# Optimization experiments

Measured on AMD Instinct MI355X. Metric: run time of the kernel, lower is better.

Reference implementation:

```python
import jax, jax.numpy as jnp
import numpy as np

N_NODES = 100000
N_EDGES = 1600000
D_IN = 64
D_OUT = 64


def setup_inputs() -> dict:
    key = jax.random.key(0)
    k1, k2, k3, k4, k5, k6 = jax.random.split(key, 6)
    x = jax.random.normal(k1, (N_NODES, D_IN), dtype=jnp.float32)
    edge_index = jax.random.randint(k2, (2, N_EDGES), 0, N_NODES, dtype=jnp.int64)
    edge_weight = jax.random.uniform(k3, (N_EDGES,), dtype=jnp.float32)
    scale = 1.0 / np.sqrt(D_IN)
    W0 = jax.random.normal(k4, (D_IN, D_OUT), dtype=jnp.float32) * scale
    W1 = jax.random.normal(k5, (D_IN, D_OUT), dtype=jnp.float32) * scale
    b = jax.random.normal(k6, (D_OUT,), dtype=jnp.float32) * 0.01
    return {"x": x, "edge_index": edge_index, "edge_weight": edge_weight,
            "W0": W0, "W1": W1, "b": b}


def reference(x, edge_index, edge_weight, W0, W1, b):
    # ChebConv K=2 with default lambda_max=2.0, sym normalization:
    # L_hat = 2L/lambda_max - I = -D^{-1/2} A D^{-1/2}
    N = x.shape[0]
    row, col = edge_index[0], edge_index[1]
    deg = jax.ops.segment_sum(edge_weight, row, num_segments=N)  # [N]
    deg_safe = jnp.where(deg > 0, deg, 1.0)
    dinv = jnp.where(deg > 0, jax.lax.rsqrt(deg_safe), 0.0)
    norm = -dinv[row] * edge_weight * dinv[col]  # [E], L_hat edge weights
    # Tx_1[i] = sum_{e: col_e = i} norm_e * x[row_e]
    Tx1 = jax.ops.segment_sum(norm[:, None] * x[row], col, num_segments=N)
    # out = lin0(Tx_0) + lin1(Tx_1) + bias
    return x @ W0 + Tx1 @ W1 + b
```

## Files before the change

### kernel.cpp

```cpp
#include <hip/hip_runtime.h>

#define N_NODES 100000
#define N_EDGES 1600000
#define D 64
#define NB 128
#define EPB (N_EDGES / NB)
#define NBUCK 3125
#define NBUCK_PAD 3136
#define NGRP 98
#define CAP 1024
#define AST 68

__device__ __forceinline__ unsigned bf16rne(float f) {
    unsigned u = __float_as_uint(f);
    return (u + 0x7FFFu + ((u >> 16) & 1u)) >> 16;
}
__global__ __launch_bounds__(256) void tobf16_kernel(const float* __restrict__ x,
                                                     ushort* __restrict__ xh) {
    int i = (blockIdx.x * 256 + threadIdx.x) * 8;
    float4 a = *(const float4*)(x + i);
    float4 b = *(const float4*)(x + i + 4);
    uint4 o;
    o.x = bf16rne(a.x) | (bf16rne(a.y) << 16);
    o.y = bf16rne(a.z) | (bf16rne(a.w) << 16);
    o.z = bf16rne(b.x) | (bf16rne(b.y) << 16);
    o.w = bf16rne(b.z) | (bf16rne(b.w) << 16);
    *(uint4*)(xh + i) = o;
}

__global__ __launch_bounds__(512) void count_kernel(const int* __restrict__ row,
                                                    const int* __restrict__ col,
                                                    int* __restrict__ matC,
                                                    int* __restrict__ matR) {
    __shared__ int cC[NBUCK_PAD];
    __shared__ int cR[NBUCK_PAD];
    int t = threadIdx.x;
    for (int j = t; j < NBUCK_PAD; j += 512) { cC[j] = 0; cR[j] = 0; }
    __syncthreads();
    int base = blockIdx.x * EPB;
    for (int i = t; i < EPB; i += 512) {
        int e = base + i;
        atomicAdd(&cC[col[e] >> 5], 1);
        atomicAdd(&cR[row[e] >> 5], 1);
    }
    __syncthreads();
    int* mc = matC + (size_t)blockIdx.x * NBUCK_PAD;
    int* mr = matR + (size_t)blockIdx.x * NBUCK_PAD;
    for (int j = t; j < NBUCK_PAD; j += 512) { mc[j] = cC[j]; mr[j] = cR[j]; }
}

__global__ __launch_bounds__(256) void blockscan_kernel(int* __restrict__ matC,
                                                        int* __restrict__ matR,
                                                        int* __restrict__ totalsC,
                                                        int* __restrict__ totalsR) {
    int which = blockIdx.x / NGRP;
    int grp   = blockIdx.x % NGRP;
    int* mat    = which ? matR : matC;
    int* totals = which ? totalsR : totalsC;
    int j0 = grp * 32;
    __shared__ int tile[NB][33];
    int t = threadIdx.x;
    int r = t >> 1;
    int h = t & 1;
    {
        const int* src = mat + (size_t)r * NBUCK_PAD + j0 + h * 16;
        int4 v0 = *(const int4*)(src + 0);
        int4 v1 = *(const int4*)(src + 4);
        int4 v2 = *(const int4*)(src + 8);
        int4 v3 = *(const int4*)(src + 12);
        int cb = h * 16;
        tile[r][cb+0]=v0.x;  tile[r][cb+1]=v0.y;  tile[r][cb+2]=v0.z;  tile[r][cb+3]=v0.w;
        tile[r][cb+4]=v1.x;  tile[r][cb+5]=v1.y;  tile[r][cb+6]=v1.z;  tile[r][cb+7]=v1.w;
        tile[r][cb+8]=v2.x;  tile[r][cb+9]=v2.y;  tile[r][cb+10]=v2.z; tile[r][cb+11]=v2.w;
        tile[r][cb+12]=v3.x; tile[r][cb+13]=v3.y; tile[r][cb+14]=v3.z; tile[r][cb+15]=v3.w;
    }
    __syncthreads();
    int g = t >> 3;
    int l = t & 7;
    int rows0 = l * 16;
    int vals[16];
    int s = 0;
    #pragma unroll
    for (int i = 0; i < 16; ++i) { vals[i] = tile[rows0 + i][g]; s += vals[i]; }
    int inc = s;
    #pragma unroll
    for (int d = 1; d < 8; d <<= 1) {
        int u = __shfl_up(inc, d, 8);
        if (l >= d) inc += u;
    }
    int excl = inc - s;
    #pragma unroll
    for (int i = 0; i < 16; ++i) { int e2 = excl; excl += vals[i]; tile[rows0 + i][g] = e2; }
    if (l == 7) totals[j0 + g] = inc;
    __syncthreads();
    {
        int* dst = mat + (size_t)r * NBUCK_PAD + j0 + h * 16;
        int cb = h * 16;
        int4 v0 = make_int4(tile[r][cb+0],  tile[r][cb+1],  tile[r][cb+2],  tile[r][cb+3]);
        int4 v1 = make_int4(tile[r][cb+4],  tile[r][cb+5],  tile[r][cb+6],  tile[r][cb+7]);
        int4 v2 = make_int4(tile[r][cb+8],  tile[r][cb+9],  tile[r][cb+10], tile[r][cb+11]);
        int4 v3 = make_int4(tile[r][cb+12], tile[r][cb+13], tile[r][cb+14], tile[r][cb+15]);
        *(int4*)(dst + 0)  = v0;
        *(int4*)(dst + 4)  = v1;
        *(int4*)(dst + 8)  = v2;
        *(int4*)(dst + 12) = v3;
    }
}

__global__ __launch_bounds__(256) void totscan_kernel(const int* __restrict__ totalsC,
                                                      int* __restrict__ bstartC,
                                                      const int* __restrict__ totalsR,
                                                      int* __restrict__ bstartR) {
    const int* tot = blockIdx.x ? totalsR : totalsC;
    int* bst       = blockIdx.x ? bstartR : bstartC;
    const int CH = (NBUCK_PAD + 255) / 256;
    __shared__ int lds[256];
    int t = threadIdx.x;
    int local[CH];
    int s = 0;
    for (int i = 0; i < CH; ++i) {
        int idx = t * CH + i;
        local[i] = (idx < NBUCK_PAD) ? tot[idx] : 0;
        s += local[i];
    }
    lds[t] = s;
    __syncthreads();
    for (int off = 1; off < 256; off <<= 1) {
        int u = (t >= off) ? lds[t - off] : 0;
        __syncthreads();
        lds[t] += u;
        __syncthreads();
    }
    int excl = (t > 0) ? lds[t - 1] : 0;
    for (int i = 0; i < CH; ++i) {
        int idx = t * CH + i;
        if (idx < NBUCK_PAD) bst[idx] = excl;
        excl += local[i];
    }
}

__global__ __launch_bounds__(512) void scatter_kernel(const int* __restrict__ row,
                                                      const int* __restrict__ col,
                                                      const float* __restrict__ w,
                                                      const int* __restrict__ matC,
                                                      const int* __restrict__ matR,
                                                      const int* __restrict__ bstartC,
                                                      const int* __restrict__ bstartR,
                                                      unsigned* __restrict__ crecs,
                                                      unsigned* __restrict__ rrecs) {
    __shared__ int cursC[NBUCK];
    __shared__ int cursR[NBUCK];
    int t = threadIdx.x;
    const int* offC = matC + (size_t)blockIdx.x * NBUCK_PAD;
    const int* offR = matR + (size_t)blockIdx.x * NBUCK_PAD;
    for (int j = t; j < NBUCK; j += 512) {
        cursC[j] = bstartC[j] + offC[j];
        cursR[j] = bstartR[j] + offR[j];
    }
    __syncthreads();
    int base = blockIdx.x * EPB;
    for (int i = t; i < EPB; i += 512) {
        int e = base + i;
        int r = row[e];
        int c = col[e];
        float we = w[e];
        unsigned wq = (unsigned)min(1023, (int)(we * 1024.f + 0.5f));
        int pC = atomicAdd(&cursC[c >> 5], 1);
        crecs[pC] = ((unsigned)r << 15) | ((unsigned)(c & 31) << 10) | wq;
        int pR = atomicAdd(&cursR[r >> 5], 1);
        rrecs[pR] = (__float_as_uint(we) & ~31u) | (unsigned)(r & 31);
    }
}

__global__ __launch_bounds__(256) void deg_kernel(const unsigned* __restrict__ rrecs,
                                                  const int* __restrict__ bstartR,
                                                  const int* __restrict__ totalsR,
                                                  float* __restrict__ dinv) {
    __shared__ float acc[32];
    int t = threadIdx.x;
    int b = blockIdx.x;
    if (t < 32) acc[t] = 0.f;
    __syncthreads();
    int base = bstartR[b];
    int cnt  = totalsR[b];
    for (int i = t; i < cnt; i += 256) {
        unsigned v = rrecs[base + i];
        atomicAdd(&acc[v & 31u], __uint_as_float(v & ~31u));
    }
    __syncthreads();
    if (t < 32) {
        float d = acc[t];
        dinv[b * 32 + t] = d > 0.f ? rsqrtf(d) : 0.f;
    }
}

#define FMA_BF16(e, u)                                                         \
    do { float cc = __int_as_float((e).y);                                     \
        acc0.x += cc * __uint_as_float((u).x << 16);                           \
        acc0.y += cc * __uint_as_float((u).x & 0xFFFF0000u);                   \
        acc0.z += cc * __uint_as_float((u).y << 16);                           \
        acc0.w += cc * __uint_as_float((u).y & 0xFFFF0000u);                   \
        acc1.x += cc * __uint_as_float((u).z << 16);                           \
        acc1.y += cc * __uint_as_float((u).z & 0xFFFF0000u);                   \
        acc1.z += cc * __uint_as_float((u).w << 16);                           \
        acc1.w += cc * __uint_as_float((u).w & 0xFFFF0000u);                   \
    } while (0)

__global__ __launch_bounds__(256) void gather_out_kernel(
        const unsigned* __restrict__ crecs, const int* __restrict__ bstartC,
        const int* __restrict__ totalsC, const float* __restrict__ dinv,
        const ushort* __restrict__ xh, const float* __restrict__ x,
        const float* __restrict__ W0, const float* __restrict__ W1,
        const float* __restrict__ bias, float* __restrict__ out) {
    __shared__ __align__(16) char smemA[32 * AST * 4];
    __shared__ __align__(16) char smemB[32 * AST * 4];
    __shared__ int cnt32[32];
    __shared__ int start32[32];
    __shared__ int cur32[32];
    int2*  srt = (int2*)smemA;
    float* xs  = (float*)smemA;
    float* ts  = (float*)smemB;

    int tid = threadIdx.x;
    int b   = blockIdx.x;
    int n0  = b * 32;
    int g   = tid >> 3;
    int j   = tid & 7;

    int base = bstartC[b];
    int cnt  = totalsC[b];

    float4 acc0 = make_float4(0.f, 0.f, 0.f, 0.f);
    float4 acc1 = make_float4(0.f, 0.f, 0.f, 0.f);
    const ushort* xhj = xh + (j << 3);

    for (int cb = 0; cb < cnt; cb += CAP) {
        int m = min(CAP, cnt - cb);
        if (tid < 32) cnt32[tid] = 0;
        __syncthreads();
        for (int i = tid; i < m; i += 256)
            atomicAdd(&cnt32[(crecs[base + cb + i] >> 10) & 31u], 1);
        __syncthreads();
        if (tid < 32) {
            int v = cnt32[tid];
            int inc = v;
            #pragma unroll
            for (int d = 1; d < 32; d <<= 1) {
                int u = __shfl_up(inc, d, 32);
                if (tid >= d) inc += u;
            }
            start32[tid] = inc - v;
            cur32[tid]   = inc - v;
        }
        __syncthreads();
        for (int i = tid; i < m; i += 256) {
            unsigned u = crecs[base + cb + i];
            int r = u >> 15;
            float cf = (float)(u & 1023u) * (1.f / 1024.f) * dinv[r];
            int p = atomicAdd(&cur32[(u >> 10) & 31u], 1);
            srt[p] = make_int2(r, __float_as_int(cf));
        }
        __syncthreads();
        int ks = start32[g];
        int ke = cur32[g];
        int k = ks;
        for (; k + 3 < ke; k += 4) {
            int2 e0 = srt[k + 0];
            int2 e1 = srt[k + 1];
            int2 e2 = srt[k + 2];
            int2 e3 = srt[k + 3];
            uint4 u0 = *(const uint4*)(xhj + ((size_t)e0.x << 6));
            uint4 u1 = *(const uint4*)(xhj + ((size_t)e1.x << 6));
            uint4 u2 = *(const uint4*)(xhj + ((size_t)e2.x << 6));
            uint4 u3 = *(const uint4*)(xhj + ((size_t)e3.x << 6));
            FMA_BF16(e0, u0);
            FMA_BF16(e1, u1);
            FMA_BF16(e2, u2);
            FMA_BF16(e3, u3);
        }
        for (; k < ke; ++k) {
            int2 e0 = srt[k];
            uint4 u0 = *(const uint4*)(xhj + ((size_t)e0.x << 6));
            FMA_BF16(e0, u0);
        }
        __syncthreads();
    }

    float dn = -dinv[n0 + g];
    float* tp = ts + g * AST + (j << 3);
    *(float4*)tp       = make_float4(dn * acc0.x, dn * acc0.y, dn * acc0.z, dn * acc0.w);
    *(float4*)(tp + 4) = make_float4(dn * acc1.x, dn * acc1.y, dn * acc1.z, dn * acc1.w);
    for (int i = tid; i < 512; i += 256) {
        int nn = i >> 4;
        int kk = (i & 15) << 2;
        *(float4*)&xs[nn * AST + kk] = *(const float4*)(x + (size_t)n0 * D + i * 4);
    }
    __syncthreads();

    int jl = j << 3;
    float4 o0 = *(const float4*)(bias + jl);
    float4 o1 = *(const float4*)(bias + jl + 4);
    for (int k = 0; k < D; k += 4) {
        float4 av = *(const float4*)&xs[g * AST + k];
        float4 tv = *(const float4*)&ts[g * AST + k];
        #pragma unroll
        for (int u = 0; u < 4; ++u) {
            float a = (u == 0) ? av.x : (u == 1) ? av.y : (u == 2) ? av.z : av.w;
            float t = (u == 0) ? tv.x : (u == 1) ? tv.y : (u == 2) ? tv.z : tv.w;
            const float4 w00 = *(const float4*)(W0 + (size_t)(k + u) * D + jl);
            const float4 w01 = *(const float4*)(W0 + (size_t)(k + u) * D + jl + 4);
            const float4 w10 = *(const float4*)(W1 + (size_t)(k + u) * D + jl);
            const float4 w11 = *(const float4*)(W1 + (size_t)(k + u) * D + jl + 4);
            o0.x += a * w00.x + t * w10.x;
            o0.y += a * w00.y + t * w10.y;
            o0.z += a * w00.z + t * w10.z;
            o0.w += a * w00.w + t * w10.w;
            o1.x += a * w01.x + t * w11.x;
            o1.y += a * w01.y + t * w11.y;
            o1.z += a * w01.z + t * w11.z;
            o1.w += a * w01.w + t * w11.w;
        }
    }
    float* op = out + (size_t)(n0 + g) * D + jl;
    *(float4*)op       = o0;
    *(float4*)(op + 4) = o1;
}

extern "C" void kernel_launch(void* const* d_in, const int* in_sizes, int n_in,
                              void* d_out, int out_size, void* d_ws, size_t ws_size,
                              hipStream_t stream) {
    const float* x    = (const float*)d_in[0];
    const int*   eidx = (const int*)d_in[1];
    const float* ew   = (const float*)d_in[2];
    const float* W0   = (const float*)d_in[3];
    const float* W1   = (const float*)d_in[4];
    const float* b    = (const float*)d_in[5];
    float* out = (float*)d_out;

    const int* row = eidx;
    const int* col = eidx + N_EDGES;

    unsigned* crecs   = (unsigned*)d_ws;
    unsigned* rrecs   = crecs + N_EDGES;
    int*      matC    = (int*)(rrecs + N_EDGES);
    int*      matR    = matC + (size_t)NB * NBUCK_PAD;
    int*      totalsC = matR + (size_t)NB * NBUCK_PAD;
    int*      bstartC = totalsC + NBUCK_PAD;
    int*      totalsR = bstartC + NBUCK_PAD;
    int*      bstartR = totalsR + NBUCK_PAD;
    float*    dinv    = (float*)(bstartR + NBUCK_PAD);
    ushort*   xh      = (ushort*)(dinv + N_NODES);

    tobf16_kernel    <<<N_NODES * D / (256 * 8), 256, 0, stream>>>(x, xh);
    count_kernel     <<<NB, 512, 0, stream>>>(row, col, matC, matR);
    blockscan_kernel <<<2 * NGRP, 256, 0, stream>>>(matC, matR, totalsC, totalsR);
    totscan_kernel   <<<2, 256, 0, stream>>>(totalsC, bstartC, totalsR, bstartR);
    scatter_kernel   <<<NB, 512, 0, stream>>>(row, col, ew, matC, matR,
                                              bstartC, bstartR, crecs, rrecs);
    deg_kernel       <<<NBUCK, 256, 0, stream>>>(rrecs, bstartR, totalsR, dinv);
    gather_out_kernel<<<NBUCK, 256, 0, stream>>>(crecs, bstartC, totalsC, dinv,
                                                 xh, x, W0, W1, b, out);
}
```

Before: 284.3 us.

## Replace count/scan bucket sort with fixed-capacity atomic buckets and atomic degree

Removes the count, two-level scan and row-bucketed scatter/degree kernels. Edges are appended with global atomics into fixed-capacity buckets (512 slots per 16 destination nodes), and degrees are accumulated with global float atomics followed by a small rsqrt kernel. The gather kernel shrinks to 16-node blocks of 128 threads and stages records in shared memory in one pass instead of a chunk loop. This cuts kernel launches and the extra passes over the edge list, but any bucket receiving more than 512 edges silently drops the excess. The float atomics also make the degree sums order-dependent.

```diff
diff --git a/kernel.cpp b/kernel.cpp
--- a/kernel.cpp
+++ b/kernel.cpp
@@ -3,12 +3,10 @@
 #define N_NODES 100000
 #define N_EDGES 1600000
 #define D 64
-#define NB 128
-#define EPB (N_EDGES / NB)
-#define NBUCK 3125
-#define NBUCK_PAD 3136
-#define NGRP 98
-#define CAP 1024
+#define BSZ 16
+#define NBUCK 6250
+#define NBUCK_PAD 6272
+#define CAPB 512
 #define AST 68
 
 __device__ __forceinline__ unsigned bf16rne(float f) {
@@ -16,8 +14,13 @@
     return (u + 0x7FFFu + ((u >> 16) & 1u)) >> 16;
 }
 __global__ __launch_bounds__(256) void tobf16_kernel(const float* __restrict__ x,
-                                                     ushort* __restrict__ xh) {
-    int i = (blockIdx.x * 256 + threadIdx.x) * 8;
+                                                     ushort* __restrict__ xh,
+                                                     float* __restrict__ deg,
+                                                     int* __restrict__ bcnt) {
+    int id = blockIdx.x * 256 + threadIdx.x;
+    if (id < N_NODES) deg[id] = 0.f;
+    if (id < NBUCK) bcnt[id] = 0;
+    int i = id * 8;
     float4 a = *(const float4*)(x + i);
     float4 b = *(const float4*)(x + i + 4);
     uint4 o;
@@ -28,170 +31,35 @@
     *(uint4*)(xh + i) = o;
 }
 
-__global__ __launch_bounds__(512) void count_kernel(const int* __restrict__ row,
-                                                    const int* __restrict__ col,
-                                                    int* __restrict__ matC,
-                                                    int* __restrict__ matR) {
-    __shared__ int cC[NBUCK_PAD];
-    __shared__ int cR[NBUCK_PAD];
-    int t = threadIdx.x;
-    for (int j = t; j < NBUCK_PAD; j += 512) { cC[j] = 0; cR[j] = 0; }
-    __syncthreads();
-    int base = blockIdx.x * EPB;
-    for (int i = t; i < EPB; i += 512) {
-        int e = base + i;
-        atomicAdd(&cC[col[e] >> 5], 1);
-        atomicAdd(&cR[row[e] >> 5], 1);
-    }
-    __syncthreads();
-    int* mc = matC + (size_t)blockIdx.x * NBUCK_PAD;
-    int* mr = matR + (size_t)blockIdx.x * NBUCK_PAD;
-    for (int j = t; j < NBUCK_PAD; j += 512) { mc[j] = cC[j]; mr[j] = cR[j]; }
-}
-
-__global__ __launch_bounds__(256) void blockscan_kernel(int* __restrict__ matC,
-                                                        int* __restrict__ matR,
-                                                        int* __restrict__ totalsC,
-                                                        int* __restrict__ totalsR) {
-    int which = blockIdx.x / NGRP;
-    int grp   = blockIdx.x % NGRP;
-    int* mat    = which ? matR : matC;
-    int* totals = which ? totalsR : totalsC;
-    int j0 = grp * 32;
-    __shared__ int tile[NB][33];
-    int t = threadIdx.x;
-    int r = t >> 1;
-    int h = t & 1;
-    {
-        const int* src = mat + (size_t)r * NBUCK_PAD + j0 + h * 16;
-        int4 v0 = *(const int4*)(src + 0);
-        int4 v1 = *(const int4*)(src + 4);
-        int4 v2 = *(const int4*)(src + 8);
-        int4 v3 = *(const int4*)(src + 12);
-        int cb = h * 16;
-        tile[r][cb+0]=v0.x;  tile[r][cb+1]=v0.y;  tile[r][cb+2]=v0.z;  tile[r][cb+3]=v0.w;
-        tile[r][cb+4]=v1.x;  tile[r][cb+5]=v1.y;  tile[r][cb+6]=v1.z;  tile[r][cb+7]=v1.w;
-        tile[r][cb+8]=v2.x;  tile[r][cb+9]=v2.y;  tile[r][cb+10]=v2.z; tile[r][cb+11]=v2.w;
-        tile[r][cb+12]=v3.x; tile[r][cb+13]=v3.y; tile[r][cb+14]=v3.z; tile[r][cb+15]=v3.w;
-    }
-    __syncthreads();
-    int g = t >> 3;
-    int l = t & 7;
-    int rows0 = l * 16;
-    int vals[16];
-    int s = 0;
-    #pragma unroll
-    for (int i = 0; i < 16; ++i) { vals[i] = tile[rows0 + i][g]; s += vals[i]; }
-    int inc = s;
-    #pragma unroll
-    for (int d = 1; d < 8; d <<= 1) {
-        int u = __shfl_up(inc, d, 8);
-        if (l >= d) inc += u;
-    }
-    int excl = inc - s;
-    #pragma unroll
-    for (int i = 0; i < 16; ++i) { int e2 = excl; excl += vals[i]; tile[rows0 + i][g] = e2; }
-    if (l == 7) totals[j0 + g] = inc;
-    __syncthreads();
-    {
-        int* dst = mat + (size_t)r * NBUCK_PAD + j0 + h * 16;
-        int cb = h * 16;
-        int4 v0 = make_int4(tile[r][cb+0],  tile[r][cb+1],  tile[r][cb+2],  tile[r][cb+3]);
-        int4 v1 = make_int4(tile[r][cb+4],  tile[r][cb+5],  tile[r][cb+6],  tile[r][cb+7]);
-        int4 v2 = make_int4(tile[r][cb+8],  tile[r][cb+9],  tile[r][cb+10], tile[r][cb+11]);
-        int4 v3 = make_int4(tile[r][cb+12], tile[r][cb+13], tile[r][cb+14], tile[r][cb+15]);
-        *(int4*)(dst + 0)  = v0;
-        *(int4*)(dst + 4)  = v1;
-        *(int4*)(dst + 8)  = v2;
-        *(int4*)(dst + 12) = v3;
-    }
-}
-
-__global__ __launch_bounds__(256) void totscan_kernel(const int* __restrict__ totalsC,
-                                                      int* __restrict__ bstartC,
-                                                      const int* __restrict__ totalsR,
-                                                      int* __restrict__ bstartR) {
-    const int* tot = blockIdx.x ? totalsR : totalsC;
-    int* bst       = blockIdx.x ? bstartR : bstartC;
-    const int CH = (NBUCK_PAD + 255) / 256;
-    __shared__ int lds[256];
-    int t = threadIdx.x;
-    int local[CH];
-    int s = 0;
-    for (int i = 0; i < CH; ++i) {
-        int idx = t * CH + i;
-        local[i] = (idx < NBUCK_PAD) ? tot[idx] : 0;
-        s += local[i];
-    }
-    lds[t] = s;
-    __syncthreads();
-    for (int off = 1; off < 256; off <<= 1) {
-        int u = (t >= off) ? lds[t - off] : 0;
-        __syncthreads();
-        lds[t] += u;
-        __syncthreads();
-    }
-    int excl = (t > 0) ? lds[t - 1] : 0;
-    for (int i = 0; i < CH; ++i) {
-        int idx = t * CH + i;
-        if (idx < NBUCK_PAD) bst[idx] = excl;
-        excl += local[i];
-    }
-}
-
-__global__ __launch_bounds__(512) void scatter_kernel(const int* __restrict__ row,
+__global__ __launch_bounds__(256) void scatter_kernel(const int* __restrict__ row,
                                                       const int* __restrict__ col,
                                                       const float* __restrict__ w,
-                                                      const int* __restrict__ matC,
-                                                      const int* __restrict__ matR,
-                                                      const int* __restrict__ bstartC,
-                                                      const int* __restrict__ bstartR,
-                                                      unsigned* __restrict__ crecs,
-                                                      unsigned* __restrict__ rrecs) {
-    __shared__ int cursC[NBUCK];
-    __shared__ int cursR[NBUCK];
-    int t = threadIdx.x;
-    const int* offC = matC + (size_t)blockIdx.x * NBUCK_PAD;
-    const int* offR = matR + (size_t)blockIdx.x * NBUCK_PAD;
-    for (int j = t; j < NBUCK; j += 512) {
-        cursC[j] = bstartC[j] + offC[j];
-        cursR[j] = bstartR[j] + offR[j];
-    }
-    __syncthreads();
-    int base = blockIdx.x * EPB;
-    for (int i = t; i < EPB; i += 512) {
-        int e = base + i;
-        int r = row[e];
-        int c = col[e];
-        float we = w[e];
-        unsigned wq = (unsigned)min(1023, (int)(we * 1024.f + 0.5f));
-        int pC = atomicAdd(&cursC[c >> 5], 1);
-        crecs[pC] = ((unsigned)r << 15) | ((unsigned)(c & 31) << 10) | wq;
-        int pR = atomicAdd(&cursR[r >> 5], 1);
-        rrecs[pR] = (__float_as_uint(we) & ~31u) | (unsigned)(r & 31);
-    }
-}
-
-__global__ __launch_bounds__(256) void deg_kernel(const unsigned* __restrict__ rrecs,
-                                                  const int* __restrict__ bstartR,
-                                                  const int* __restrict__ totalsR,
-                                                  float* __restrict__ dinv) {
-    __shared__ float acc[32];
-    int t = threadIdx.x;
-    int b = blockIdx.x;
-    if (t < 32) acc[t] = 0.f;
-    __syncthreads();
-    int base = bstartR[b];
-    int cnt  = totalsR[b];
-    for (int i = t; i < cnt; i += 256) {
-        unsigned v = rrecs[base + i];
-        atomicAdd(&acc[v & 31u], __uint_as_float(v & ~31u));
-    }
-    __syncthreads();
-    if (t < 32) {
-        float d = acc[t];
-        dinv[b * 32 + t] = d > 0.f ? rsqrtf(d) : 0.f;
-    }
+                                                      float* __restrict__ deg,
+                                                      int* __restrict__ bcnt,
+                                                      unsigned* __restrict__ crecs) {
+    int e = blockIdx.x * 256 + threadIdx.x;
+    int r = row[e];
+    int c = col[e];
+    float we = w[e];
+    atomicAdd(&deg[r], we);
+    unsigned wq = (unsigned)min(1023, (int)(we * 1024.f + 0.5f));
+    int b = c >> 4;
+    int p = atomicAdd(&bcnt[b], 1);
+    if (p < CAPB)
+        crecs[((size_t)b << 9) + p] = ((unsigned)r << 14) | ((unsigned)(c & 15) << 10) | wq;
+}
+
+__global__ __launch_bounds__(256) void dinv_kernel(const float* __restrict__ deg,
+                                                   float* __restrict__ dinv) {
+    int i = (blockIdx.x * 256 + threadIdx.x) * 4;
+    if (i >= N_NODES) return;
+    float4 d = *(const float4*)(deg + i);
+    float4 o;
+    o.x = d.x > 0.f ? rsqrtf(d.x) : 0.f;
+    o.y = d.y > 0.f ? rsqrtf(d.y) : 0.f;
+    o.z = d.z > 0.f ? rsqrtf(d.z) : 0.f;
+    o.w = d.w > 0.f ? rsqrtf(d.w) : 0.f;
+    *(float4*)(dinv + i) = o;
 }
 
 #define FMA_BF16(e, u)                                                         \
@@ -206,91 +74,92 @@
         acc1.w += cc * __uint_as_float((u).w & 0xFFFF0000u);                   \
     } while (0)
 
-__global__ __launch_bounds__(256) void gather_out_kernel(
-        const unsigned* __restrict__ crecs, const int* __restrict__ bstartC,
-        const int* __restrict__ totalsC, const float* __restrict__ dinv,
-        const ushort* __restrict__ xh, const float* __restrict__ x,
-        const float* __restrict__ W0, const float* __restrict__ W1,
-        const float* __restrict__ bias, float* __restrict__ out) {
-    __shared__ __align__(16) char smemA[32 * AST * 4];
-    __shared__ __align__(16) char smemB[32 * AST * 4];
-    __shared__ int cnt32[32];
-    __shared__ int start32[32];
-    __shared__ int cur32[32];
-    int2*  srt = (int2*)smemA;
-    float* xs  = (float*)smemA;
-    float* ts  = (float*)smemB;
+__global__ __launch_bounds__(128, 8) void gather_out_kernel(
+        const unsigned* __restrict__ crecs, const int* __restrict__ bcnt,
+        const float* __restrict__ dinv, const ushort* __restrict__ xh,
+        const float* __restrict__ x, const float* __restrict__ W0,
+        const float* __restrict__ W1, const float* __restrict__ bias,
+        float* __restrict__ out) {
+    __shared__ __align__(16) char smemA[BSZ * AST * 4];
+    __shared__ __align__(16) char smemB[BSZ * AST * 4];
+    __shared__ int cnt16[16];
+    __shared__ int start16[16];
+    __shared__ int cur16[16];
+    int2*     srt = (int2*)smemA;
+    float*    xs  = (float*)smemA;
+    unsigned* stg = (unsigned*)smemB;
+    float*    ts  = (float*)smemB;
 
     int tid = threadIdx.x;
     int b   = blockIdx.x;
-    int n0  = b * 32;
+    int n0  = b * BSZ;
     int g   = tid >> 3;
     int j   = tid & 7;
 
-    int base = bstartC[b];
-    int cnt  = totalsC[b];
+    size_t base = (size_t)b * CAPB;
+    int cnt = min(bcnt[b], CAPB);
+
+    if (tid < 16) cnt16[tid] = 0;
+    __syncthreads();
+    for (int i = tid; i < cnt; i += 128) {
+        unsigned u = crecs[base + i];
+        stg[i] = u;
+        atomicAdd(&cnt16[(u >> 10) & 15u], 1);
+    }
+    __syncthreads();
+    if (tid < 16) {
+        int v = cnt16[tid];
+        int inc = v;
+        #pragma unroll
+        for (int d = 1; d < 16; d <<= 1) {
+            int u = __shfl_up(inc, d, 16);
+            if (tid >= d) inc += u;
+        }
+        start16[tid] = inc - v;
+        cur16[tid]   = inc - v;
+    }
+    __syncthreads();
+    for (int i = tid; i < cnt; i += 128) {
+        unsigned u = stg[i];
+        int r = u >> 14;
+        float cf = (float)(u & 1023u) * (1.f / 1024.f) * dinv[r];
+        int p = atomicAdd(&cur16[(u >> 10) & 15u], 1);
+        srt[p] = make_int2(r, __float_as_int(cf));
+    }
+    __syncthreads();
 
     float4 acc0 = make_float4(0.f, 0.f, 0.f, 0.f);
     float4 acc1 = make_float4(0.f, 0.f, 0.f, 0.f);
     const ushort* xhj = xh + (j << 3);
-
-    for (int cb = 0; cb < cnt; cb += CAP) {
-        int m = min(CAP, cnt - cb);
-        if (tid < 32) cnt32[tid] = 0;
-        __syncthreads();
-        for (int i = tid; i < m; i += 256)
-            atomicAdd(&cnt32[(crecs[base + cb + i] >> 10) & 31u], 1);
-        __syncthreads();
-        if (tid < 32) {
-            int v = cnt32[tid];
-            int inc = v;
-            #pragma unroll
-            for (int d = 1; d < 32; d <<= 1) {
-                int u = __shfl_up(inc, d, 32);
-                if (tid >= d) inc += u;
-            }
-            start32[tid] = inc - v;
-            cur32[tid]   = inc - v;
-        }
-        __syncthreads();
-        for (int i = tid; i < m; i += 256) {
-            unsigned u = crecs[base + cb + i];
-            int r = u >> 15;
-            float cf = (float)(u & 1023u) * (1.f / 1024.f) * dinv[r];
-            int p = atomicAdd(&cur32[(u >> 10) & 31u], 1);
-            srt[p] = make_int2(r, __float_as_int(cf));
-        }
-        __syncthreads();
-        int ks = start32[g];
-        int ke = cur32[g];
-        int k = ks;
-        for (; k + 3 < ke; k += 4) {
-            int2 e0 = srt[k + 0];
-            int2 e1 = srt[k + 1];
-            int2 e2 = srt[k + 2];
-            int2 e3 = srt[k + 3];
-            uint4 u0 = *(const uint4*)(xhj + ((size_t)e0.x << 6));
-            uint4 u1 = *(const uint4*)(xhj + ((size_t)e1.x << 6));
-            uint4 u2 = *(const uint4*)(xhj + ((size_t)e2.x << 6));
-            uint4 u3 = *(const uint4*)(xhj + ((size_t)e3.x << 6));
-            FMA_BF16(e0, u0);
-            FMA_BF16(e1, u1);
-            FMA_BF16(e2, u2);
-            FMA_BF16(e3, u3);
-        }
-        for (; k < ke; ++k) {
-            int2 e0 = srt[k];
-            uint4 u0 = *(const uint4*)(xhj + ((size_t)e0.x << 6));
-            FMA_BF16(e0, u0);
-        }
-        __syncthreads();
-    }
+    int ks = start16[g];
+    int ke = cur16[g];
+    int k = ks;
+    for (; k + 3 < ke; k += 4) {
+        int2 e0 = srt[k + 0];
+        int2 e1 = srt[k + 1];
+        int2 e2 = srt[k + 2];
+        int2 e3 = srt[k + 3];
+        uint4 u0 = *(const uint4*)(xhj + ((size_t)e0.x << 6));
+        uint4 u1 = *(const uint4*)(xhj + ((size_t)e1.x << 6));
+        uint4 u2 = *(const uint4*)(xhj + ((size_t)e2.x << 6));
+        uint4 u3 = *(const uint4*)(xhj + ((size_t)e3.x << 6));
+        FMA_BF16(e0, u0);
+        FMA_BF16(e1, u1);
+        FMA_BF16(e2, u2);
+        FMA_BF16(e3, u3);
+    }
+    for (; k < ke; ++k) {
+        int2 e0 = srt[k];
+        uint4 u0 = *(const uint4*)(xhj + ((size_t)e0.x << 6));
+        FMA_BF16(e0, u0);
+    }
+    __syncthreads();
 
     float dn = -dinv[n0 + g];
     float* tp = ts + g * AST + (j << 3);
     *(float4*)tp       = make_float4(dn * acc0.x, dn * acc0.y, dn * acc0.z, dn * acc0.w);
     *(float4*)(tp + 4) = make_float4(dn * acc1.x, dn * acc1.y, dn * acc1.z, dn * acc1.w);
-    for (int i = tid; i < 512; i += 256) {
+    for (int i = tid; i < 256; i += 128) {
         int nn = i >> 4;
         int kk = (i & 15) << 2;
         *(float4*)&xs[nn * AST + kk] = *(const float4*)(x + (size_t)n0 * D + i * 4);
@@ -300,17 +169,17 @@
     int jl = j << 3;
     float4 o0 = *(const float4*)(bias + jl);
     float4 o1 = *(const float4*)(bias + jl + 4);
-    for (int k = 0; k < D; k += 4) {
-        float4 av = *(const float4*)&xs[g * AST + k];
-        float4 tv = *(const float4*)&ts[g * AST + k];
+    for (int k2 = 0; k2 < D; k2 += 4) {
+        float4 av = *(const float4*)&xs[g * AST + k2];
+        float4 tv = *(const float4*)&ts[g * AST + k2];
         #pragma unroll
         for (int u = 0; u < 4; ++u) {
             float a = (u == 0) ? av.x : (u == 1) ? av.y : (u == 2) ? av.z : av.w;
             float t = (u == 0) ? tv.x : (u == 1) ? tv.y : (u == 2) ? tv.z : tv.w;
-            const float4 w00 = *(const float4*)(W0 + (size_t)(k + u) * D + jl);
-            const float4 w01 = *(const float4*)(W0 + (size_t)(k + u) * D + jl + 4);
-            const float4 w10 = *(const float4*)(W1 + (size_t)(k + u) * D + jl);
-            const float4 w11 = *(const float4*)(W1 + (size_t)(k + u) * D + jl + 4);
+            const float4 w00 = *(const float4*)(W0 + (size_t)(k2 + u) * D + jl);
+            const float4 w01 = *(const float4*)(W0 + (size_t)(k2 + u) * D + jl + 4);
+            const float4 w10 = *(const float4*)(W1 + (size_t)(k2 + u) * D + jl);
+            const float4 w11 = *(const float4*)(W1 + (size_t)(k2 + u) * D + jl + 4);
             o0.x += a * w00.x + t * w10.x;
             o0.y += a * w00.y + t * w10.y;
             o0.z += a * w00.z + t * w10.z;
@@ -340,24 +209,14 @@
     const int* row = eidx;
     const int* col = eidx + N_EDGES;
 
-    unsigned* crecs   = (unsigned*)d_ws;
-    unsigned* rrecs   = crecs + N_EDGES;
-    int*      matC    = (int*)(rrecs + N_EDGES);
-    int*      matR    = matC + (size_t)NB * NBUCK_PAD;
-    int*      totalsC = matR + (size_t)NB * NBUCK_PAD;
-    int*      bstartC = totalsC + NBUCK_PAD;
-    int*      totalsR = bstartC + NBUCK_PAD;
-    int*      bstartR = totalsR + NBUCK_PAD;
-    float*    dinv    = (float*)(bstartR + NBUCK_PAD);
-    ushort*   xh      = (ushort*)(dinv + N_NODES);
-
-    tobf16_kernel    <<<N_NODES * D / (256 * 8), 256, 0, stream>>>(x, xh);
-    count_kernel     <<<NB, 512, 0, stream>>>(row, col, matC, matR);
-    blockscan_kernel <<<2 * NGRP, 256, 0, stream>>>(matC, matR, totalsC, totalsR);
-    totscan_kernel   <<<2, 256, 0, stream>>>(totalsC, bstartC, totalsR, bstartR);
-    scatter_kernel   <<<NB, 512, 0, stream>>>(row, col, ew, matC, matR,
-                                              bstartC, bstartR, crecs, rrecs);
-    deg_kernel       <<<NBUCK, 256, 0, stream>>>(rrecs, bstartR, totalsR, dinv);
-    gather_out_kernel<<<NBUCK, 256, 0, stream>>>(crecs, bstartC, totalsC, dinv,
-                                                 xh, x, W0, W1, b, out);
-}
+    unsigned* crecs = (unsigned*)d_ws;
+    float*    deg   = (float*)(crecs + (size_t)NBUCK * CAPB);
+    float*    dinv  = deg + N_NODES;
+    int*      bcnt  = (int*)(dinv + N_NODES);
+    ushort*   xh    = (ushort*)(bcnt + NBUCK_PAD);
+
+    tobf16_kernel    <<<N_NODES * D / (256 * 8), 256, 0, stream>>>(x, xh, deg, bcnt);
+    scatter_kernel   <<<N_EDGES / 256, 256, 0, stream>>>(row, col, ew, deg, bcnt, crecs);
+    dinv_kernel      <<<(N_NODES / 4 + 255) / 256, 256, 0, stream>>>(deg, dinv);
+    gather_out_kernel<<<NBUCK, 128, 0, stream>>>(crecs, bcnt, dinv, xh, x, W0, W1, b, out);
+}
```

After: 376.0 us. +32.2%, slower.

## Compute degree via global atomics into four replicas instead of row bucket sort

Applied to the files above, without the earlier changes.

Drops the row-side bucket counting, scan, record scatter and per-bucket degree reduction. Degree is now accumulated with global float atomicAdd into four replicated arrays chosen by block index; the arrays are zeroed inside the bf16 conversion kernel and summed plus rsqrt'd in a small new kernel. This removes the second radix-style pass over all edges and its record traffic, at the cost of 1.6M contended global atomics and nondeterministic float summation order.

```diff
diff --git a/kernel.cpp b/kernel.cpp
--- a/kernel.cpp
+++ b/kernel.cpp
@@ -16,8 +16,11 @@
     return (u + 0x7FFFu + ((u >> 16) & 1u)) >> 16;
 }
 __global__ __launch_bounds__(256) void tobf16_kernel(const float* __restrict__ x,
-                                                     ushort* __restrict__ xh) {
-    int i = (blockIdx.x * 256 + threadIdx.x) * 8;
+                                                     ushort* __restrict__ xh,
+                                                     float* __restrict__ deg4) {
+    int id = blockIdx.x * 256 + threadIdx.x;
+    if (id < 4 * N_NODES) deg4[id] = 0.f;
+    int i = id * 8;
     float4 a = *(const float4*)(x + i);
     float4 b = *(const float4*)(x + i + 4);
     uint4 o;
@@ -30,40 +33,35 @@
 
 __global__ __launch_bounds__(512) void count_kernel(const int* __restrict__ row,
                                                     const int* __restrict__ col,
-                                                    int* __restrict__ matC,
-                                                    int* __restrict__ matR) {
+                                                    const float* __restrict__ w,
+                                                    float* __restrict__ deg4,
+                                                    int* __restrict__ matC) {
     __shared__ int cC[NBUCK_PAD];
-    __shared__ int cR[NBUCK_PAD];
     int t = threadIdx.x;
-    for (int j = t; j < NBUCK_PAD; j += 512) { cC[j] = 0; cR[j] = 0; }
+    for (int j = t; j < NBUCK_PAD; j += 512) cC[j] = 0;
     __syncthreads();
     int base = blockIdx.x * EPB;
+    float* dg = deg4 + (size_t)(blockIdx.x & 3) * N_NODES;
     for (int i = t; i < EPB; i += 512) {
         int e = base + i;
+        atomicAdd(&dg[row[e]], w[e]);
         atomicAdd(&cC[col[e] >> 5], 1);
-        atomicAdd(&cR[row[e] >> 5], 1);
     }
     __syncthreads();
     int* mc = matC + (size_t)blockIdx.x * NBUCK_PAD;
-    int* mr = matR + (size_t)blockIdx.x * NBUCK_PAD;
-    for (int j = t; j < NBUCK_PAD; j += 512) { mc[j] = cC[j]; mr[j] = cR[j]; }
+    for (int j = t; j < NBUCK_PAD; j += 512) mc[j] = cC[j];
 }
 
 __global__ __launch_bounds__(256) void blockscan_kernel(int* __restrict__ matC,
-                                                        int* __restrict__ matR,
-                                                        int* __restrict__ totalsC,
-                                                        int* __restrict__ totalsR) {
-    int which = blockIdx.x / NGRP;
-    int grp   = blockIdx.x % NGRP;
-    int* mat    = which ? matR : matC;
-    int* totals = which ? totalsR : totalsC;
+                                                        int* __restrict__ totalsC) {
+    int grp = blockIdx.x;
     int j0 = grp * 32;
     __shared__ int tile[NB][33];
     int t = threadIdx.x;
     int r = t >> 1;
     int h = t & 1;
     {
-        const int* src = mat + (size_t)r * NBUCK_PAD + j0 + h * 16;
+        const int* src = matC + (size_t)r * NBUCK_PAD + j0 + h * 16;
         int4 v0 = *(const int4*)(src + 0);
         int4 v1 = *(const int4*)(src + 4);
         int4 v2 = *(const int4*)(src + 8);
@@ -91,10 +89,10 @@
     int excl = inc - s;
     #pragma unroll
     for (int i = 0; i < 16; ++i) { int e2 = excl; excl += vals[i]; tile[rows0 + i][g] = e2; }
-    if (l == 7) totals[j0 + g] = inc;
+    if (l == 7) totalsC[j0 + g] = inc;
     __syncthreads();
     {
-        int* dst = mat + (size_t)r * NBUCK_PAD + j0 + h * 16;
+        int* dst = matC + (size_t)r * NBUCK_PAD + j0 + h * 16;
         int cb = h * 16;
         int4 v0 = make_int4(tile[r][cb+0],  tile[r][cb+1],  tile[r][cb+2],  tile[r][cb+3]);
         int4 v1 = make_int4(tile[r][cb+4],  tile[r][cb+5],  tile[r][cb+6],  tile[r][cb+7]);
@@ -108,11 +106,7 @@
 }
 
 __global__ __launch_bounds__(256) void totscan_kernel(const int* __restrict__ totalsC,
-                                                      int* __restrict__ bstartC,
-                                                      const int* __restrict__ totalsR,
-                                                      int* __restrict__ bstartR) {
-    const int* tot = blockIdx.x ? totalsR : totalsC;
-    int* bst       = blockIdx.x ? bstartR : bstartC;
+                                                      int* __restrict__ bstartC) {
     const int CH = (NBUCK_PAD + 255) / 256;
     __shared__ int lds[256];
     int t = threadIdx.x;
@@ -120,7 +114,7 @@
     int s = 0;
     for (int i = 0; i < CH; ++i) {
         int idx = t * CH + i;
-        local[i] = (idx < NBUCK_PAD) ? tot[idx] : 0;
+        local[i] = (idx < NBUCK_PAD) ? totalsC[idx] : 0;
         s += local[i];
     }
     lds[t] = s;
@@ -134,7 +128,7 @@
     int excl = (t > 0) ? lds[t - 1] : 0;
     for (int i = 0; i < CH; ++i) {
         int idx = t * CH + i;
-        if (idx < NBUCK_PAD) bst[idx] = excl;
+        if (idx < NBUCK_PAD) bstartC[idx] = excl;
         excl += local[i];
     }
 }
@@ -143,20 +137,12 @@
                                                       const int* __restrict__ col,
                                                       const float* __restrict__ w,
                                                       const int* __restrict__ matC,
-                                                      const int* __restrict__ matR,
                                                       const int* __restrict__ bstartC,
-                                                      const int* __restrict__ bstartR,
-                                                      unsigned* __restrict__ crecs,
-                                                      unsigned* __restrict__ rrecs) {
+                                                      unsigned* __restrict__ crecs) {
     __shared__ int cursC[NBUCK];
-    __shared__ int cursR[NBUCK];
     int t = threadIdx.x;
     const int* offC = matC + (size_t)blockIdx.x * NBUCK_PAD;
-    const int* offR = matR + (size_t)blockIdx.x * NBUCK_PAD;
-    for (int j = t; j < NBUCK; j += 512) {
-        cursC[j] = bstartC[j] + offC[j];
-        cursR[j] = bstartR[j] + offR[j];
-    }
+    for (int j = t; j < NBUCK; j += 512) cursC[j] = bstartC[j] + offC[j];
     __syncthreads();
     int base = blockIdx.x * EPB;
     for (int i = t; i < EPB; i += 512) {
@@ -167,31 +153,27 @@
         unsigned wq = (unsigned)min(1023, (int)(we * 1024.f + 0.5f));
         int pC = atomicAdd(&cursC[c >> 5], 1);
         crecs[pC] = ((unsigned)r << 15) | ((unsigned)(c & 31) << 10) | wq;
-        int pR = atomicAdd(&cursR[r >> 5], 1);
-        rrecs[pR] = (__float_as_uint(we) & ~31u) | (unsigned)(r & 31);
-    }
-}
-
-__global__ __launch_bounds__(256) void deg_kernel(const unsigned* __restrict__ rrecs,
-                                                  const int* __restrict__ bstartR,
-                                                  const int* __restrict__ totalsR,
-                                                  float* __restrict__ dinv) {
-    __shared__ float acc[32];
-    int t = threadIdx.x;
-    int b = blockIdx.x;
-    if (t < 32) acc[t] = 0.f;
-    __syncthreads();
-    int base = bstartR[b];
-    int cnt  = totalsR[b];
-    for (int i = t; i < cnt; i += 256) {
-        unsigned v = rrecs[base + i];
-        atomicAdd(&acc[v & 31u], __uint_as_float(v & ~31u));
-    }
-    __syncthreads();
-    if (t < 32) {
-        float d = acc[t];
-        dinv[b * 32 + t] = d > 0.f ? rsqrtf(d) : 0.f;
-    }
+    }
+}
+
+__global__ __launch_bounds__(256) void dinv_kernel(const float* __restrict__ deg4,
+                                                   float* __restrict__ dinv) {
+    int i = (blockIdx.x * 256 + threadIdx.x) * 4;
+    if (i >= N_NODES) return;
+    float4 a = *(const float4*)(deg4 + i);
+    float4 b = *(const float4*)(deg4 + N_NODES + i);
+    float4 c = *(const float4*)(deg4 + 2 * N_NODES + i);
+    float4 d = *(const float4*)(deg4 + 3 * N_NODES + i);
+    float sx = a.x + b.x + c.x + d.x;
+    float sy = a.y + b.y + c.y + d.y;
+    float sz = a.z + b.z + c.z + d.z;
+    float sw = a.w + b.w + c.w + d.w;
+    float4 o;
+    o.x = sx > 0.f ? rsqrtf(sx) : 0.f;
+    o.y = sy > 0.f ? rsqrtf(sy) : 0.f;
+    o.z = sz > 0.f ? rsqrtf(sz) : 0.f;
+    o.w = sw > 0.f ? rsqrtf(sw) : 0.f;
+    *(float4*)(dinv + i) = o;
 }
 
 #define FMA_BF16(e, u)                                                         \
@@ -341,23 +323,19 @@
     const int* col = eidx + N_EDGES;
 
     unsigned* crecs   = (unsigned*)d_ws;
-    unsigned* rrecs   = crecs + N_EDGES;
-    int*      matC    = (int*)(rrecs + N_EDGES);
-    int*      matR    = matC + (size_t)NB * NBUCK_PAD;
-    int*      totalsC = matR + (size_t)NB * NBUCK_PAD;
+    int*      matC    = (int*)(crecs + N_EDGES);
+    int*      totalsC = matC + (size_t)NB * NBUCK_PAD;
     int*      bstartC = totalsC + NBUCK_PAD;
-    int*      totalsR = bstartC + NBUCK_PAD;
-    int*      bstartR = totalsR + NBUCK_PAD;
-    float*    dinv    = (float*)(bstartR + NBUCK_PAD);
+    float*    deg4    = (float*)(bstartC + NBUCK_PAD);
+    float*    dinv    = deg4 + 4 * N_NODES;
     ushort*   xh      = (ushort*)(dinv + N_NODES);
 
-    tobf16_kernel    <<<N_NODES * D / (256 * 8), 256, 0, stream>>>(x, xh);
-    count_kernel     <<<NB, 512, 0, stream>>>(row, col, matC, matR);
-    blockscan_kernel <<<2 * NGRP, 256, 0, stream>>>(matC, matR, totalsC, totalsR);
-    totscan_kernel   <<<2, 256, 0, stream>>>(totalsC, bstartC, totalsR, bstartR);
-    scatter_kernel   <<<NB, 512, 0, stream>>>(row, col, ew, matC, matR,
-                                              bstartC, bstartR, crecs, rrecs);
-    deg_kernel       <<<NBUCK, 256, 0, stream>>>(rrecs, bstartR, totalsR, dinv);
+    tobf16_kernel    <<<N_NODES * D / (256 * 8), 256, 0, stream>>>(x, xh, deg4);
+    count_kernel     <<<NB, 512, 0, stream>>>(row, col, ew, deg4, matC);
+    blockscan_kernel <<<NGRP, 256, 0, stream>>>(matC, totalsC);
+    totscan_kernel   <<<1, 256, 0, stream>>>(totalsC, bstartC);
+    scatter_kernel   <<<NB, 512, 0, stream>>>(row, col, ew, matC, bstartC, crecs);
+    dinv_kernel      <<<98, 256, 0, stream>>>(deg4, dinv);
     gather_out_kernel<<<NBUCK, 256, 0, stream>>>(crecs, bstartC, totalsC, dinv,
                                                  xh, x, W0, W1, b, out);
 }
```

After: 326.7 us. 14.9% more time.
